# Performance work log

Hardware: AMD Instinct MI355X
Metric: run time of the kernel (lower is better)

The kernel has to match this reference:

```python
import jax, jax.numpy as jnp
import numpy as np

N = 100000   # nodes
E = 800000   # edges
D = 128      # uniform hidden width
L = 3        # number of SAGE layers (len(hidden_channels)-1)
EPS = 1e-5   # BatchNorm eps


def setup_inputs() -> dict:
    key = jax.random.key(0)
    ks = jax.random.split(key, 7)
    s = 1.0 / np.sqrt(D)
    x = jax.random.normal(ks[0], (N, D), jnp.float32)
    edge_index = jax.random.randint(ks[1], (2, E), 0, N)
    Wl = jax.random.normal(ks[2], (L, D, D), jnp.float32) * s  # neighbor-branch weight (out,in)
    Wr = jax.random.normal(ks[3], (L, D, D), jnp.float32) * s  # root-branch weight (out,in)
    b = jax.random.normal(ks[4], (L, D), jnp.float32) * 0.01   # bias (lin_l only, PyG default)
    gamma = 1.0 + 0.1 * jax.random.normal(ks[5], (L, D), jnp.float32)
    beta = 0.1 * jax.random.normal(ks[6], (L, D), jnp.float32)
    return {"x": x, "edge_index": edge_index, "Wl": Wl, "Wr": Wr, "b": b,
            "gamma": gamma, "beta": beta}


def _sage(x, src, dst, Wl, Wr, b):
    # PyG SAGEConv: out = lin_l(mean_{j->i} x_j) + lin_r(x_i)
    agg = jax.ops.segment_sum(x[src], dst, num_segments=N)          # [N, D]
    cnt = jax.ops.segment_sum(jnp.ones((src.shape[0], 1), x.dtype), dst,
                              num_segments=N)                        # [N, 1]
    agg = agg / jnp.maximum(cnt, 1.0)  # mean; isolated nodes stay 0
    return agg @ Wl.T + x @ Wr.T + b


def _bn(x, g, be):
    # BatchNorm1d over the node axis, batch statistics, biased variance
    m = jnp.mean(x, axis=0)
    v = jnp.var(x, axis=0)
    return g * (x - m) * jax.lax.rsqrt(v + EPS) + be


def reference(x, edge_index, Wl, Wr, b, gamma, beta):
    src, dst = edge_index[0], edge_index[1]
    # hidden layers: SAGEConv -> ELU -> (dropout, eval no-op) -> BatchNorm
    for i in range(L - 1):
        h = jax.nn.elu(_sage(x, src, dst, Wl[i], Wr[i], b[i]))
        x = _bn(h, gamma[i], beta[i])
    # final layer: SAGEConv -> BatchNorm (no ELU/dropout)
    x = _bn(_sage(x, src, dst, Wl[L - 1], Wr[L - 1], b[L - 1]), gamma[L - 1], beta[L - 1])
    return x
```

## Files before the change

kernel.cpp:

```cpp
#include <hip/hip_runtime.h>
#include <hip/hip_bf16.h>

#define N_NODES 100000
#define N_EDGES 800000
#define DD 128
#define TILE 32
#define NBLK 3125
#define NSCAN1 391
#define EPSV 1e-5f
#define ECAP 768

typedef short bf16x8 __attribute__((ext_vector_type(8)));
typedef float f32x4 __attribute__((ext_vector_type(4)));

__device__ __forceinline__ short f2bf(float f) {
    unsigned u = __float_as_uint(f);
    unsigned r = (u + 0x7fffu + ((u >> 16) & 1u)) >> 16;
    return (short)r;
}
__device__ __forceinline__ float bf2f(short s) {
    return __uint_as_float(((unsigned)(unsigned short)s) << 16);
}

__global__ void k_setup(const float* __restrict__ x, short* __restrict__ xbf,
                        const int* __restrict__ dst, int* __restrict__ cnt) {
    int i = blockIdx.x * 256 + threadIdx.x;
    if (i < N_NODES * DD / 8) {
        f32x4 v0 = *(const f32x4*)(x + (size_t)i * 8);
        f32x4 v1 = *(const f32x4*)(x + (size_t)i * 8 + 4);
        bf16x8 t;
        t[0] = f2bf(v0.x); t[1] = f2bf(v0.y); t[2] = f2bf(v0.z); t[3] = f2bf(v0.w);
        t[4] = f2bf(v1.x); t[5] = f2bf(v1.y); t[6] = f2bf(v1.z); t[7] = f2bf(v1.w);
        *(bf16x8*)&xbf[(size_t)i * 8] = t;
    }
    if (i < N_EDGES) atomicAdd(&cnt[dst[i]], 1);
}

__global__ void k_scan1(const int* __restrict__ cnt, int* __restrict__ off,
                        int* __restrict__ bsums) {
    __shared__ int s[256];
    int i = blockIdx.x * 256 + threadIdx.x;
    int t = threadIdx.x;
    s[t] = (i < N_NODES) ? cnt[i] : 0;
    __syncthreads();
    for (int d = 1; d < 256; d <<= 1) {
        int x = 0;
        if (t >= d) x = s[t - d];
        __syncthreads();
        s[t] += x;
        __syncthreads();
    }
    if (i < N_NODES) off[i + 1] = s[t];
    if (t == 255) bsums[blockIdx.x] = s[255];
}

__global__ void k_scan2(int* __restrict__ bsums) {
    __shared__ int s[512];
    int t = threadIdx.x;
    s[t] = (t < NSCAN1) ? bsums[t] : 0;
    __syncthreads();
    for (int d = 1; d < 512; d <<= 1) {
        int x = 0;
        if (t >= d) x = s[t - d];
        __syncthreads();
        s[t] += x;
        __syncthreads();
    }
    if (t < NSCAN1) bsums[t] = s[t];
}

__global__ void k_scan3(int* __restrict__ off, const int* __restrict__ bsums) {
    int i = blockIdx.x * 256 + threadIdx.x;
    int add = (blockIdx.x > 0) ? bsums[blockIdx.x - 1] : 0;
    if (i < N_NODES) off[i + 1] += add;
    if (i == 0) off[0] = 0;
}

__global__ void k_fill(const int* __restrict__ src, const int* __restrict__ dst,
                       const int* __restrict__ off, int* __restrict__ cur,
                       int* __restrict__ elist) {
    int e = blockIdx.x * 256 + threadIdx.x;
    if (e < N_EDGES) {
        int d = dst[e];
        int p = atomicSub(&cur[d], 1);
        elist[off[d] + p - 1] = src[e];
    }
}

__global__ void k_fold(const float* __restrict__ wl, const float* __restrict__ wr,
                       const float* __restrict__ b, const float* __restrict__ aff,
                       int use_aff,
                       short* __restrict__ wblo, short* __restrict__ wbro,
                       float* __restrict__ bias_base, float* __restrict__ bias_deg) {
    int o = blockIdx.x;
    int k = threadIdx.x;
    float a = use_aff ? aff[k] : 1.f;
    float c = use_aff ? aff[128 + k] : 0.f;
    float vl = wl[o * DD + k], vr = wr[o * DD + k];
    wblo[o * DD + k] = f2bf(vl * a);
    wbro[o * DD + k] = f2bf(vr * a);
    __shared__ float s1[128], s2[128];
    s1[k] = c * vr; s2[k] = c * vl;
    __syncthreads();
    for (int d = 64; d > 0; d >>= 1) {
        if (k < d) { s1[k] += s1[k + d]; s2[k] += s2[k + d]; }
        __syncthreads();
    }
    if (k == 0) {
        bias_base[o] = b[o] + s1[0];
        bias_deg[o] = s2[0];
    }
}

template <bool ELU_ON>
__global__ __launch_bounds__(256, 6) void k_sage(
    const short* __restrict__ xbf,
    const int* __restrict__ off, const int* __restrict__ elist,
    const short* __restrict__ wl, const short* __restrict__ wr,
    const float* __restrict__ bias_base, const float* __restrict__ bias_deg,
    short* __restrict__ hout, float* __restrict__ partials)
{
    __shared__ short agg_t[TILE * 128];
    __shared__ int sdeg[TILE];
    __shared__ float sstat[4 * 128];
    __shared__ int soff[TILE + 1];
    __shared__ int eidx[ECAP];
    const int tid = threadIdx.x;
    const int wu = __builtin_amdgcn_readfirstlane(tid >> 6);
    const int l = tid & 63;
    const int base = blockIdx.x * TILE;
    const int qw = l >> 4;
    const int ll = l & 15;

    if (tid < TILE + 1) soff[tid] = off[min(base + tid, N_NODES)];
    __syncthreads();
    const int ebase = soff[0];
    const int etot = soff[TILE] - ebase;
    const bool ovf = etot > ECAP;
    for (int k = tid; k < (ovf ? 0 : etot); k += 256) eidx[k] = elist[ebase + k];
    __syncthreads();
    const int* ep = ovf ? (elist + ebase) : (const int*)eidx;

#pragma unroll
    for (int q = 0; q < 2; ++q) {
        const int m = wu * 8 + q * 4 + qw;
        const int ea = soff[m] - ebase;
        const int eA = soff[m + 1] - ebase;
        const int deg = eA - ea;
        float acc[8];
#pragma unroll
        for (int j = 0; j < 8; ++j) acc[j] = 0.f;

        int e = ea;
        bool val0 = e < eA, val1 = e + 1 < eA;
        bf16x8 v0{}, v1{};
        if (val0) v0 = *(const bf16x8*)(xbf + (size_t)ep[e] * DD + 8 * ll);
        if (val1) v1 = *(const bf16x8*)(xbf + (size_t)ep[e + 1] * DD + 8 * ll);
        while (__any((int)(val0 || val1))) {
            int en = e + 2;
            bool nv0 = en < eA, nv1 = en + 1 < eA;
            bf16x8 w0{}, w1{};
            if (nv0) w0 = *(const bf16x8*)(xbf + (size_t)ep[en] * DD + 8 * ll);
            if (nv1) w1 = *(const bf16x8*)(xbf + (size_t)ep[en + 1] * DD + 8 * ll);
            if (val0) {
#pragma unroll
                for (int j = 0; j < 8; ++j) acc[j] += bf2f(v0[j]);
            }
            if (val1) {
#pragma unroll
                for (int j = 0; j < 8; ++j) acc[j] += bf2f(v1[j]);
            }
            v0 = w0; v1 = w1; val0 = nv0; val1 = nv1; e = en;
        }

        float inv = deg > 0 ? 1.f / (float)deg : 0.f;
        bf16x8 t;
#pragma unroll
        for (int j = 0; j < 8; ++j) t[j] = f2bf(acc[j] * inv);
        *(bf16x8*)&agg_t[m * DD + ((8 * ll) ^ ((m & 7) << 3))] = t;
        if (ll == 0) sdeg[m] = deg;
    }
    __syncthreads();

    const int p = wu >> 1;
    const int half = wu & 1;
    f32x4 acc[4];
#pragma unroll
    for (int nb = 0; nb < 4; ++nb) acc[nb] = f32x4{0.f, 0.f, 0.f, 0.f};
    const int mrow = p * 16 + (l & 15);
    const int kg = (l >> 4) * 8;
    const int nloc = l & 15;
    const int groot = min(base + mrow, N_NODES - 1);
#pragma unroll
    for (int ks = 0; ks < 4; ++ks) {
        int kk = ks * 32 + kg;
        int sw = kk ^ ((mrow & 7) << 3);
        bf16x8 aa = *(const bf16x8*)&agg_t[mrow * DD + sw];
        bf16x8 ax = *(const bf16x8*)(xbf + (size_t)groot * DD + kk);
#pragma unroll
        for (int nb = 0; nb < 4; ++nb) {
            int n = half * 64 + nb * 16 + nloc;
            bf16x8 bl = *(const bf16x8*)&wl[n * DD + kk];
            bf16x8 br = *(const bf16x8*)&wr[n * DD + kk];
            acc[nb] = __builtin_amdgcn_mfma_f32_16x16x32_bf16(aa, bl, acc[nb], 0, 0, 0);
            acc[nb] = __builtin_amdgcn_mfma_f32_16x16x32_bf16(ax, br, acc[nb], 0, 0, 0);
        }
    }
    __syncthreads();

    int degf[4];
#pragma unroll
    for (int r = 0; r < 4; ++r) degf[r] = sdeg[p * 16 + (l >> 4) * 4 + r];

    float colS[4], colQ[4];
#pragma unroll
    for (int nb = 0; nb < 4; ++nb) {
        int n = half * 64 + nb * 16 + nloc;
        float bb = bias_base[n];
        float bd = bias_deg[n];
        float cs = 0.f, cq = 0.f;
#pragma unroll
        for (int r = 0; r < 4; ++r) {
            int m = p * 16 + (l >> 4) * 4 + r;
            int g = base + m;
            float hv = acc[nb][r] + bb + (degf[r] > 0 ? bd : 0.f);
            if (ELU_ON) hv = hv > 0.f ? hv : expm1f(hv);
            agg_t[m * DD + (n ^ ((m & 7) << 3))] = f2bf(hv);
            float hm = (g < N_NODES) ? hv : 0.f;
            cs += hm;
            cq += hm * hm;
        }
        colS[nb] = cs; colQ[nb] = cq;
    }
#pragma unroll
    for (int nb = 0; nb < 4; ++nb) {
        colS[nb] += __shfl_xor(colS[nb], 16, 64);
        colS[nb] += __shfl_xor(colS[nb], 32, 64);
        colQ[nb] += __shfl_xor(colQ[nb], 16, 64);
        colQ[nb] += __shfl_xor(colQ[nb], 32, 64);
    }
    if (l < 16) {
#pragma unroll
        for (int nb = 0; nb < 4; ++nb) {
            sstat[wu * 128 + nb * 16 + l]      = colS[nb];
            sstat[wu * 128 + 64 + nb * 16 + l] = colQ[nb];
        }
    }
    __syncthreads();

#pragma unroll
    for (int k = 0; k < 2; ++k) {
        int idx = (k * 256 + tid) * 8;
        int m = idx >> 7, c = idx & 127;
        int g = base + m;
        if (g < N_NODES) {
            bf16x8 v = *(const bf16x8*)&agg_t[m * DD + (c ^ ((m & 7) << 3))];
            *(bf16x8*)&hout[(size_t)g * DD + c] = v;
        }
    }
    {
        int f = tid & 127;
        int part = tid >> 7;
        int hsel = f >> 6;
        int cw = part * 64 + (f & 63);
        float v = 0.f;
#pragma unroll
        for (int pr = 0; pr < 2; ++pr) v += sstat[(2 * pr + hsel) * 128 + cw];
        partials[blockIdx.x * 256 + tid] = v;
    }
}

__global__ void k_reduce(const float* __restrict__ partials,
                         const float* __restrict__ gamma, const float* __restrict__ beta,
                         float* __restrict__ aff) {
    int f = blockIdx.x;
    int t = threadIdx.x;
    float s = 0.f, q = 0.f;
    for (int i = t; i < NBLK; i += 256) {
        s += partials[i * 256 + f];
        q += partials[i * 256 + 128 + f];
    }
    __shared__ float rs[256], rq[256];
    rs[t] = s; rq[t] = q;
    __syncthreads();
    for (int d = 128; d > 0; d >>= 1) {
        if (t < d) { rs[t] += rs[t + d]; rq[t] += rq[t + d]; }
        __syncthreads();
    }
    if (t == 0) {
        float mean = rs[0] / (float)N_NODES;
        float var = rq[0] / (float)N_NODES - mean * mean;
        float a = gamma[f] * rsqrtf(var + EPSV);
        aff[f] = a;
        aff[128 + f] = beta[f] - mean * a;
    }
}

__global__ void k_apply(const short* __restrict__ hin, const float* __restrict__ aff,
                        float* __restrict__ out) {
    int i = blockIdx.x * 256 + threadIdx.x;
    if (i < N_NODES * DD / 8) {
        bf16x8 v = *(const bf16x8*)(hin + (size_t)i * 8);
        int f = (i * 8) & 127;
        f32x4 a0 = *(const f32x4*)(aff + f);
        f32x4 a1 = *(const f32x4*)(aff + f + 4);
        f32x4 c0 = *(const f32x4*)(aff + 128 + f);
        f32x4 c1 = *(const f32x4*)(aff + 128 + f + 4);
        f32x4 o0, o1;
        o0.x = bf2f(v[0]) * a0.x + c0.x; o0.y = bf2f(v[1]) * a0.y + c0.y;
        o0.z = bf2f(v[2]) * a0.z + c0.z; o0.w = bf2f(v[3]) * a0.w + c0.w;
        o1.x = bf2f(v[4]) * a1.x + c1.x; o1.y = bf2f(v[5]) * a1.y + c1.y;
        o1.z = bf2f(v[6]) * a1.z + c1.z; o1.w = bf2f(v[7]) * a1.w + c1.w;
        *(f32x4*)(out + (size_t)i * 8) = o0;
        *(f32x4*)(out + (size_t)i * 8 + 4) = o1;
    }
}

extern "C" void kernel_launch(void* const* d_in, const int* in_sizes, int n_in,
                              void* d_out, int out_size, void* d_ws, size_t ws_size,
                              hipStream_t stream) {
    const float* x     = (const float*)d_in[0];
    const int*   ei    = (const int*)d_in[1];
    const float* Wl    = (const float*)d_in[2];
    const float* Wr    = (const float*)d_in[3];
    const float* b     = (const float*)d_in[4];
    const float* gamma = (const float*)d_in[5];
    const float* beta  = (const float*)d_in[6];
    float* out = (float*)d_out;

    char* ws = (char*)d_ws;
    int*   off      = (int*)(ws + 0);
    int*   cnt      = (int*)(ws + 400128);
    int*   elist    = (int*)(ws + 800256);
    int*   bsums    = (int*)(ws + 4000256);
    float* partials = (float*)(ws + 4002304);
    float* affine   = (float*)(ws + 7202304);
    short* wbl      = (short*)(ws + 7203328);
    short* wbr      = (short*)(ws + 7236096);
    float* biasb    = (float*)(ws + 7268864);
    float* biasd    = (float*)(ws + 7269376);
    short* bufA     = (short*)(ws + 7269888);
    short* bufB     = (short*)(ws + 32869888);

    const int* src = ei;
    const int* dst = ei + N_EDGES;

    hipMemsetAsync(cnt, 0, N_NODES * sizeof(int), stream);
    k_setup<<<(N_NODES * DD / 8 + 255) / 256, 256, 0, stream>>>(x, bufA, dst, cnt);
    k_scan1<<<NSCAN1, 256, 0, stream>>>(cnt, off, bsums);
    k_scan2<<<1, 512, 0, stream>>>(bsums);
    k_scan3<<<NSCAN1, 256, 0, stream>>>(off, bsums);
    k_fill<<<(N_EDGES + 255) / 256, 256, 0, stream>>>(src, dst, off, cnt, elist);

    k_fold<<<128, 128, 0, stream>>>(Wl, Wr, b, affine, 0, wbl, wbr, biasb, biasd);
    k_sage<true><<<NBLK, 256, 0, stream>>>(bufA, off, elist, wbl, wbr,
                                           biasb, biasd, bufB, partials);
    k_reduce<<<128, 256, 0, stream>>>(partials, gamma, beta, affine);

    k_fold<<<128, 128, 0, stream>>>(Wl + DD * DD, Wr + DD * DD, b + DD, affine, 1,
                                    wbl, wbr, biasb, biasd);
    k_sage<true><<<NBLK, 256, 0, stream>>>(bufB, off, elist, wbl, wbr,
                                           biasb, biasd, bufA, partials);
    k_reduce<<<128, 256, 0, stream>>>(partials, gamma + DD, beta + DD, affine);

    k_fold<<<128, 128, 0, stream>>>(Wl + 2 * DD * DD, Wr + 2 * DD * DD, b + 2 * DD,
                                    affine, 1, wbl, wbr, biasb, biasd);
    k_sage<false><<<NBLK, 256, 0, stream>>>(bufA, off, elist, wbl, wbr,
                                            biasb, biasd, bufB, partials);
    k_reduce<<<128, 256, 0, stream>>>(partials, gamma + 2 * DD, beta + 2 * DD, affine);

    k_apply<<<(N_NODES * DD / 8 + 255) / 256, 256, 0, stream>>>(bufB, affine, out);
}
```

Baseline: 408.2 us.

## Balance edge aggregation across quarter-waves with packed dst tags and LDS atomics

The edge list now packs the low five bits of the destination node into each source index. Each wave's edges are split evenly across its four 16-lane groups instead of giving each group whole rows, which removes load imbalance from degree skew. Partial row sums are flushed into an fp32 LDS tile with atomicAdd, then converted to swizzled bf16 in a separate pass, and degree is recomputed from the offsets. This adds LDS atomics, a zero-init pass, extra barriers and larger fp32 shared storage, which may reduce occupancy.

```diff
diff --git a/kernel.cpp b/kernel.cpp
--- a/kernel.cpp
+++ b/kernel.cpp
@@ -9,6 +9,7 @@
 #define NSCAN1 391
 #define EPSV 1e-5f
 #define ECAP 768
+#define SRCMASK 0x1FFFF
 
 typedef short bf16x8 __attribute__((ext_vector_type(8)));
 typedef float f32x4 __attribute__((ext_vector_type(4)));
@@ -83,7 +84,7 @@
     if (e < N_EDGES) {
         int d = dst[e];
         int p = atomicSub(&cur[d], 1);
-        elist[off[d] + p - 1] = src[e];
+        elist[off[d] + p - 1] = src[e] | ((d & 31) << 17);
     }
 }
 
@@ -120,9 +121,7 @@
     const float* __restrict__ bias_base, const float* __restrict__ bias_deg,
     short* __restrict__ hout, float* __restrict__ partials)
 {
-    __shared__ short agg_t[TILE * 128];
-    __shared__ int sdeg[TILE];
-    __shared__ float sstat[4 * 128];
+    __shared__ float aggf[TILE * 128];
     __shared__ int soff[TILE + 1];
     __shared__ int eidx[ECAP];
     const int tid = threadIdx.x;
@@ -133,6 +132,12 @@
     const int ll = l & 15;
 
     if (tid < TILE + 1) soff[tid] = off[min(base + tid, N_NODES)];
+    {
+        f32x4* az = (f32x4*)aggf;
+        f32x4 z{0.f, 0.f, 0.f, 0.f};
+#pragma unroll
+        for (int k = 0; k < 4; ++k) az[k * 256 + tid] = z;
+    }
     __syncthreads();
     const int ebase = soff[0];
     const int etot = soff[TILE] - ebase;
@@ -141,44 +146,71 @@
     __syncthreads();
     const int* ep = ovf ? (elist + ebase) : (const int*)eidx;
 
-#pragma unroll
-    for (int q = 0; q < 2; ++q) {
-        const int m = wu * 8 + q * 4 + qw;
-        const int ea = soff[m] - ebase;
-        const int eA = soff[m + 1] - ebase;
-        const int deg = eA - ea;
+    {
+        const int wrb = wu * 8;
+        const int eAw = soff[wrb] - ebase;
+        const int eBw = soff[wrb + 8] - ebase;
+        const int cs = (eBw - eAw + 3) >> 2;
+        const int ce0 = eAw + qw * cs;
+        const int ce1 = min(ce0 + cs, eBw);
+
         float acc[8];
 #pragma unroll
         for (int j = 0; j < 8; ++j) acc[j] = 0.f;
-
-        int e = ea;
-        bool val0 = e < eA, val1 = e + 1 < eA;
-        bf16x8 v0{}, v1{};
-        if (val0) v0 = *(const bf16x8*)(xbf + (size_t)ep[e] * DD + 8 * ll);
-        if (val1) v1 = *(const bf16x8*)(xbf + (size_t)ep[e + 1] * DD + 8 * ll);
-        while (__any((int)(val0 || val1))) {
-            int en = e + 2;
-            bool nv0 = en < eA, nv1 = en + 1 < eA;
-            bf16x8 w0{}, w1{};
-            if (nv0) w0 = *(const bf16x8*)(xbf + (size_t)ep[en] * DD + 8 * ll);
-            if (nv1) w1 = *(const bf16x8*)(xbf + (size_t)ep[en + 1] * DD + 8 * ll);
-            if (val0) {
-#pragma unroll
-                for (int j = 0; j < 8; ++j) acc[j] += bf2f(v0[j]);
-            }
-            if (val1) {
-#pragma unroll
-                for (int j = 0; j < 8; ++j) acc[j] += bf2f(v1[j]);
-            }
-            v0 = w0; v1 = w1; val0 = nv0; val1 = nv1; e = en;
+        int mcur = -1;
+        bf16x8 v0{}, v1{}, v2{}, v3{};
+        int mr0 = 0, mr1 = 0, mr2 = 0, mr3 = 0;
+
+#define GLOAD(pk) (*(const bf16x8*)(xbf + (size_t)((pk) & SRCMASK) * DD + 8 * ll))
+#define ISSUE(d) { int i_ = ce0 + d; if (i_ < ce1) { int pk = ep[i_]; \
+        mr##d = pk >> 17; v##d = GLOAD(pk); } }
+        ISSUE(0) ISSUE(1) ISSUE(2) ISSUE(3)
+#define FLUSH() { int fb = mcur * DD + ((8 * ll) ^ ((mcur & 3) << 3)); \
+        _Pragma("unroll") \
+        for (int j = 0; j < 8; ++j) { atomicAdd(&aggf[fb + j], acc[j]); acc[j] = 0.f; } }
+#define STEP(d) { int i_ = ib + d; if (i_ < ce1) { \
+        if (mr##d != mcur) { if (mcur >= 0) FLUSH(); mcur = mr##d; } \
+        _Pragma("unroll") \
+        for (int j = 0; j < 8; ++j) acc[j] += bf2f(v##d[j]); \
+        int en = i_ + 4; if (en < ce1) { int pk = ep[en]; \
+            mr##d = pk >> 17; v##d = GLOAD(pk); } } }
+
+        for (int ib = ce0; ib < ce1; ib += 4) {
+            STEP(0) STEP(1) STEP(2) STEP(3)
         }
-
+        if (mcur >= 0) FLUSH();
+#undef STEP
+#undef FLUSH
+#undef ISSUE
+#undef GLOAD
+    }
+    __syncthreads();
+
+    short* agg_t = (short*)aggf;
+    {
+        int cm = tid >> 3;
+        int g0 = (tid & 7) * 2;
+        int deg = soff[cm + 1] - soff[cm];
         float inv = deg > 0 ? 1.f / (float)deg : 0.f;
-        bf16x8 t;
-#pragma unroll
-        for (int j = 0; j < 8; ++j) t[j] = f2bf(acc[j] * inv);
-        *(bf16x8*)&agg_t[m * DD + ((8 * ll) ^ ((m & 7) << 3))] = t;
-        if (ll == 0) sdeg[m] = deg;
+        const float* rowp = aggf + cm * DD;
+        int ga = g0 ^ (cm & 3);
+        int gb = (g0 + 1) ^ (cm & 3);
+        f32x4 a0 = *(const f32x4*)(rowp + ga * 8);
+        f32x4 a1 = *(const f32x4*)(rowp + ga * 8 + 4);
+        f32x4 b0 = *(const f32x4*)(rowp + gb * 8);
+        f32x4 b1 = *(const f32x4*)(rowp + gb * 8 + 4);
+        __syncthreads();
+        bf16x8 ta, tb;
+        ta[0] = f2bf(a0.x * inv); ta[1] = f2bf(a0.y * inv);
+        ta[2] = f2bf(a0.z * inv); ta[3] = f2bf(a0.w * inv);
+        ta[4] = f2bf(a1.x * inv); ta[5] = f2bf(a1.y * inv);
+        ta[6] = f2bf(a1.z * inv); ta[7] = f2bf(a1.w * inv);
+        tb[0] = f2bf(b0.x * inv); tb[1] = f2bf(b0.y * inv);
+        tb[2] = f2bf(b0.z * inv); tb[3] = f2bf(b0.w * inv);
+        tb[4] = f2bf(b1.x * inv); tb[5] = f2bf(b1.y * inv);
+        tb[6] = f2bf(b1.z * inv); tb[7] = f2bf(b1.w * inv);
+        *(bf16x8*)&agg_t[cm * DD + ((g0 ^ (cm & 7)) << 3)] = ta;
+        *(bf16x8*)&agg_t[cm * DD + (((g0 + 1) ^ (cm & 7)) << 3)] = tb;
     }
     __syncthreads();
 
@@ -208,9 +240,13 @@
     }
     __syncthreads();
 
+    float* sstat = (float*)eidx;
     int degf[4];
 #pragma unroll
-    for (int r = 0; r < 4; ++r) degf[r] = sdeg[p * 16 + (l >> 4) * 4 + r];
+    for (int r = 0; r < 4; ++r) {
+        int mr_ = p * 16 + (l >> 4) * 4 + r;
+        degf[r] = soff[mr_ + 1] - soff[mr_];
+    }
 
     float colS[4], colQ[4];
 #pragma unroll
```

New measurement: 514.1 us. +25.9%, slower.
